# Optimization experiments

Measured on AMD Instinct MI355X. Metric: run time of the kernel, lower is better.

Reference implementation:

```python
import jax, jax.numpy as jnp
import numpy as np

QMAX = 127.0  # 2**(bits-1) - 1 for bits=8, signed symmetric


def _quantize_signed_symmetric(t):
    # per-tensor symmetric: scale = max|t| / qmax, q = clamp(round(t/scale))
    scale = jnp.max(jnp.abs(t)) / QMAX
    q = jnp.clip(jnp.round(t / scale), -QMAX, QMAX)
    return q, scale


def setup_inputs() -> dict:
    key = jax.random.key(0)
    k1, k2, k3 = jax.random.split(key, 3)
    N, D_IN, D_OUT = 16384, 1024, 1024
    x = jax.random.normal(k1, (N, D_IN), dtype=jnp.float32)
    weight = jax.random.normal(k2, (D_OUT, D_IN), dtype=jnp.float32) * 0.02
    bias = jax.random.normal(k3, (D_OUT,), dtype=jnp.float32) * 0.01
    return {"x": x, "weight": weight, "bias": bias}


def reference(x, weight, bias):
    # weight quantization (cached in torch; recomputed here, same math)
    qw, w_scale = _quantize_signed_symmetric(weight)
    qw_t = qw.astype(jnp.int32).T            # [D_IN, D_OUT]
    # activation quantization
    qx, x_scale = _quantize_signed_symmetric(x)
    qx = qx.astype(jnp.int32)                # [N, D_IN]
    # int32 matmul, then per-tensor dequant + bias
    acc = qx @ qw_t                          # int32 [N, D_OUT]
    y = acc.astype(jnp.float32) * (x_scale * w_scale)
    return y + bias
```

## Files before the change

### kernel.cpp

```cpp
#include <hip/hip_runtime.h>

#define QMAX 127.0f

typedef int int4v __attribute__((ext_vector_type(4)));
typedef float float4v __attribute__((ext_vector_type(4)));

__device__ __forceinline__ float amax4(float4 v) {
    return fmaxf(fmaxf(fabsf(v.x), fabsf(v.y)), fmaxf(fabsf(v.z), fabsf(v.w)));
}
__device__ __forceinline__ int qone(float v, float s) {
    float q = fminf(fmaxf(rintf(v / s), -QMAX), QMAX);
    return (int)q;
}
__device__ __forceinline__ int qpack4(float4 v, float s) {
    return (qone(v.x, s) & 255) | ((qone(v.y, s) & 255) << 8) |
           ((qone(v.z, s) & 255) << 16) | ((qone(v.w, s) & 255) << 24);
}

__global__ void absmax2_kernel(const float4* __restrict__ px, int n4x,
                               const float4* __restrict__ pw, int n4w,
                               int gx, int* __restrict__ amax) {
    const float4* p; int n4; int* out; int nb, bid;
    if ((int)blockIdx.x < gx) { p = px; n4 = n4x; out = amax + 0; nb = gx; bid = blockIdx.x; }
    else { p = pw; n4 = n4w; out = amax + 1; nb = gridDim.x - gx; bid = blockIdx.x - gx; }
    const int S = nb * blockDim.x;
    int i = bid * blockDim.x + threadIdx.x;
    float a = 0.f, b = 0.f, c = 0.f, d = 0.f;
    for (; i + 3 * S < n4; i += 4 * S) {
        float4 v0 = p[i];
        float4 v1 = p[i + S];
        float4 v2 = p[i + 2 * S];
        float4 v3 = p[i + 3 * S];
        a = fmaxf(a, amax4(v0));
        b = fmaxf(b, amax4(v1));
        c = fmaxf(c, amax4(v2));
        d = fmaxf(d, amax4(v3));
    }
    for (; i < n4; i += S) a = fmaxf(a, amax4(p[i]));
    float m = fmaxf(fmaxf(a, b), fmaxf(c, d));
    for (int off = 32; off; off >>= 1) m = fmaxf(m, __shfl_down(m, off, 64));
    __shared__ float sm[4];
    if ((threadIdx.x & 63) == 0) sm[threadIdx.x >> 6] = m;
    __syncthreads();
    if (threadIdx.x == 0) {
        float bm = fmaxf(fmaxf(sm[0], sm[1]), fmaxf(sm[2], sm[3]));
        atomicMax(out, (int)__float_as_uint(bm));
    }
}

__global__ void quantw_kernel(const float4* __restrict__ sw, int4v* __restrict__ dw,
                              int n16w, int kshift, int KC,
                              const int* __restrict__ amax) {
    const float scale = __uint_as_float((unsigned)amax[1]) / QMAX;
    const int stride = gridDim.x * blockDim.x;
    for (int i = blockIdx.x * blockDim.x + threadIdx.x; i < n16w; i += stride) {
        float4 v0 = sw[4 * i + 0];
        float4 v1 = sw[4 * i + 1];
        float4 v2 = sw[4 * i + 2];
        float4 v3 = sw[4 * i + 3];
        int4v o = { qpack4(v0, scale), qpack4(v1, scale),
                    qpack4(v2, scale), qpack4(v3, scale) };
        const int n = i >> kshift;
        const int kg = i & ((1 << kshift) - 1);
        const int kc = kg >> 2, q = kg & 3;
        const int g = n >> 4, r = n & 15;
        dw[(g * KC + kc) * 64 + q * 16 + r] = o;
    }
}

__global__ __launch_bounds__(1024, 4) void gemm_i8_kernel(
        const float* __restrict__ x, const char* __restrict__ qb,
        const float4* __restrict__ bias4, const int* __restrict__ amax,
        float* __restrict__ out, int M, int N, int K) {
    extern __shared__ char sA[];

    const int KC = K >> 6;
    const int CH = KC >> 2;
    const int tid = threadIdx.x;
    const int lane = tid & 63;
    const int wv = tid >> 6;
    const int m0 = blockIdx.x * 64;

    const int si = wv >> 2;
    const int skcl = wv & 3;
    const int srow = m0 + si * 16 + (lane & 15);
    const int sk0 = skcl * 64 + (lane >> 4) * 16;
    const float4* sbase4 = (const float4*)(x + (size_t)srow * K + sk0);
    const int sslot = si * 256 + skcl * 64 + lane;

    const float xs = __uint_as_float((unsigned)amax[0]) / QMAX;

    const char* bbase = qb + (size_t)(wv * 4) * KC * 1024 + lane * 16;

#define LOADB(Bb, kc)                                                        \
    do { _Pragma("unroll") for (int j = 0; j < 4; ++j)                       \
        Bb[j] = *(const int4v*)(bbase + ((size_t)j * KC + (kc)) * 1024);     \
    } while (0)
#define LOADA2(kcl, ih)                                                      \
    do { _Pragma("unroll") for (int i = 0; i < 2; ++i)                       \
        Af[i] = sAv[((ih) * 2 + i) * 256 + (kcl) * 64 + lane];               \
    } while (0)
#define MF2(Bb, ih)                                                          \
    do { _Pragma("unroll") for (int j = 0; j < 4; ++j)                       \
        _Pragma("unroll") for (int i = 0; i < 2; ++i)                        \
            acc[j][(ih) * 2 + i] = __builtin_amdgcn_mfma_i32_16x16x64_i8(    \
                Bb[j], Af[i], acc[j][(ih) * 2 + i], 0, 0, 0);                \
    } while (0)
#define KCQUAD(Bb0, Bb1, kcl0, kcl1)                                         \
    do { LOADA2(kcl0, 0); MF2(Bb0, 0); LOADA2(kcl0, 1); MF2(Bb0, 1);         \
         LOADA2(kcl1, 0); MF2(Bb1, 0); LOADA2(kcl1, 1); MF2(Bb1, 1);         \
    } while (0)
#define ISSUEA(h) do { xr0 = sbase4[(h) * 64]; xr1 = sbase4[(h) * 64 + 1]; } while (0)
#define ISSUEB(h) do { xr0 = sbase4[(h) * 64 + 2]; xr1 = sbase4[(h) * 64 + 3]; } while (0)

    float4 xr0, xr1;
    int qa0, qa1;
    int4v B0[4], B1[4], Af[2];

    ISSUEA(0);
    LOADB(B0, 0);
    qa0 = qpack4(xr0, xs); qa1 = qpack4(xr1, xs);
    ISSUEB(0);
    {
        int4v o = { qa0, qa1, qpack4(xr0, xs), qpack4(xr1, xs) };
        ((int4v*)sA)[sslot] = o;
    }
    __syncthreads();

    int4v acc[4][4];
    const int4v zero = {0, 0, 0, 0};
#pragma unroll
    for (int j = 0; j < 4; ++j)
#pragma unroll
        for (int i = 0; i < 4; ++i) acc[j][i] = zero;

#pragma unroll 1
    for (int h = 0; h < CH - 1; ++h) {
        const int4v* sAv = (const int4v*)(sA + (h & 1) * 16384);
        const int kc0 = h * 4;
        ISSUEA(h + 1);
        LOADB(B1, kc0 + 1);
        KCQUAD(B0, B1, 0, 1);
        LOADB(B0, kc0 + 2);
        qa0 = qpack4(xr0, xs); qa1 = qpack4(xr1, xs);
        ISSUEB(h + 1);
        LOADB(B1, kc0 + 3);
        KCQUAD(B0, B1, 2, 3);
        LOADB(B0, kc0 + 4);
        {
            int4v o = { qa0, qa1, qpack4(xr0, xs), qpack4(xr1, xs) };
            ((int4v*)(sA + ((h + 1) & 1) * 16384))[sslot] = o;
        }
        __syncthreads();
    }
    {
        const int4v* sAv = (const int4v*)(sA + ((CH - 1) & 1) * 16384);
        const int kc0 = (CH - 1) * 4;
        LOADB(B1, kc0 + 1);
        KCQUAD(B0, B1, 0, 1);
        LOADB(B0, kc0 + 2);
        LOADB(B1, kc0 + 3);
        KCQUAD(B0, B1, 2, 3);
    }

    const float sc = xs * (__uint_as_float((unsigned)amax[1]) / QMAX);
    const int quad = lane >> 4;
    const int rbase = m0 + (lane & 15);
    const int cb4 = wv * 16;
#pragma unroll
    for (int j = 0; j < 4; ++j) {
        const float4 bv = bias4[cb4 + j * 4 + quad];
#pragma unroll
        for (int i = 0; i < 4; ++i) {
            const int row = rbase + i * 16;
            float4v v;
            v[0] = (float)acc[j][i][0] * sc + bv.x;
            v[1] = (float)acc[j][i][1] * sc + bv.y;
            v[2] = (float)acc[j][i][2] * sc + bv.z;
            v[3] = (float)acc[j][i][3] * sc + bv.w;
            *((float4v*)(out + (size_t)row * N) + cb4 + j * 4 + quad) = v;
        }
    }
}

extern "C" void kernel_launch(void* const* d_in, const int* in_sizes, int n_in,
                              void* d_out, int out_size, void* d_ws, size_t ws_size,
                              hipStream_t stream) {
    const float* x = (const float*)d_in[0];
    const float* w = (const float*)d_in[1];
    const float* bias = (const float*)d_in[2];
    float* out = (float*)d_out;

    const int xn = in_sizes[0];
    const int wn = in_sizes[1];
    const int N = in_sizes[2];
    const int K = wn / N;
    const int M = xn / K;
    const int KC = K >> 6;
    const int kshift = __builtin_ctz(K >> 4);

    int* amax = (int*)d_ws;
    char* qw = (char*)d_ws + 1024;

    const int GAX = 2048, GAW = 256;
    absmax2_kernel<<<GAX + GAW, 256, 0, stream>>>(
        (const float4*)x, xn / 4, (const float4*)w, wn / 4, GAX, amax);

    quantw_kernel<<<256, 256, 0, stream>>>(
        (const float4*)w, (int4v*)qw, wn / 16, kshift, KC, amax);

    gemm_i8_kernel<<<M / 64, 1024, 32768, stream>>>(
        x, qw, (const float4*)bias, amax, out, M, N, K);
}
```

Baseline: 190.2 us.

## Halve waves per block and give each wave a 128-column output tile

The GEMM block drops from 16 waves to 8, and each wave now computes a 64x128 output tile (8x4 accumulators) in place of 64x64. The K staging step shrinks from 256 to 128 per LDS double-buffer stage, which halves shared memory. Each A fragment read from LDS now feeds 8 B fragments, so more MFMAs run per LDS load and per barrier. The cost is about twice the register pressure per wave and lower occupancy (launch bounds 512,2), which may reduce latency hiding for the global B loads.

```diff
diff --git a/kernel.cpp b/kernel.cpp
--- a/kernel.cpp
+++ b/kernel.cpp
@@ -68,54 +68,51 @@
     }
 }
 
-__global__ __launch_bounds__(1024, 4) void gemm_i8_kernel(
+__global__ __launch_bounds__(512, 2) void gemm_i8_kernel(
         const float* __restrict__ x, const char* __restrict__ qb,
         const float4* __restrict__ bias4, const int* __restrict__ amax,
         float* __restrict__ out, int M, int N, int K) {
     extern __shared__ char sA[];
 
     const int KC = K >> 6;
-    const int CH = KC >> 2;
+    const int NCH = KC >> 1;
     const int tid = threadIdx.x;
     const int lane = tid & 63;
     const int wv = tid >> 6;
     const int m0 = blockIdx.x * 64;
 
-    const int si = wv >> 2;
-    const int skcl = wv & 3;
+    const int si = wv >> 1;
+    const int skcl = wv & 1;
     const int srow = m0 + si * 16 + (lane & 15);
     const int sk0 = skcl * 64 + (lane >> 4) * 16;
     const float4* sbase4 = (const float4*)(x + (size_t)srow * K + sk0);
-    const int sslot = si * 256 + skcl * 64 + lane;
+    const int sslot = si * 128 + skcl * 64 + lane;
 
     const float xs = __uint_as_float((unsigned)amax[0]) / QMAX;
 
-    const char* bbase = qb + (size_t)(wv * 4) * KC * 1024 + lane * 16;
+    const char* bbase = qb + (size_t)(wv * 8) * KC * 1024 + lane * 16;
 
 #define LOADB(Bb, kc)                                                        \
-    do { _Pragma("unroll") for (int j = 0; j < 4; ++j)                       \
+    do { _Pragma("unroll") for (int j = 0; j < 8; ++j)                       \
         Bb[j] = *(const int4v*)(bbase + ((size_t)j * KC + (kc)) * 1024);     \
     } while (0)
-#define LOADA2(kcl, ih)                                                      \
-    do { _Pragma("unroll") for (int i = 0; i < 2; ++i)                       \
-        Af[i] = sAv[((ih) * 2 + i) * 256 + (kcl) * 64 + lane];               \
+#define LOADA(Af, buf, kcl)                                                  \
+    do { const int4v* sAv = (const int4v*)(sA + (buf) * 8192);               \
+        _Pragma("unroll") for (int i = 0; i < 4; ++i)                        \
+            Af[i] = sAv[i * 128 + (kcl) * 64 + lane];                        \
     } while (0)
-#define MF2(Bb, ih)                                                          \
-    do { _Pragma("unroll") for (int j = 0; j < 4; ++j)                       \
-        _Pragma("unroll") for (int i = 0; i < 2; ++i)                        \
-            acc[j][(ih) * 2 + i] = __builtin_amdgcn_mfma_i32_16x16x64_i8(    \
-                Bb[j], Af[i], acc[j][(ih) * 2 + i], 0, 0, 0);                \
+#define MF(Bb, Af)                                                           \
+    do { _Pragma("unroll") for (int j = 0; j < 8; ++j)                       \
+        _Pragma("unroll") for (int i = 0; i < 4; ++i)                        \
+            acc[j][i] = __builtin_amdgcn_mfma_i32_16x16x64_i8(               \
+                Bb[j], Af[i], acc[j][i], 0, 0, 0);                           \
     } while (0)
-#define KCQUAD(Bb0, Bb1, kcl0, kcl1)                                         \
-    do { LOADA2(kcl0, 0); MF2(Bb0, 0); LOADA2(kcl0, 1); MF2(Bb0, 1);         \
-         LOADA2(kcl1, 0); MF2(Bb1, 0); LOADA2(kcl1, 1); MF2(Bb1, 1);         \
-    } while (0)
-#define ISSUEA(h) do { xr0 = sbase4[(h) * 64]; xr1 = sbase4[(h) * 64 + 1]; } while (0)
-#define ISSUEB(h) do { xr0 = sbase4[(h) * 64 + 2]; xr1 = sbase4[(h) * 64 + 3]; } while (0)
+#define ISSUEA(h) do { xr0 = sbase4[(h) * 32]; xr1 = sbase4[(h) * 32 + 1]; } while (0)
+#define ISSUEB(h) do { xr0 = sbase4[(h) * 32 + 2]; xr1 = sbase4[(h) * 32 + 3]; } while (0)
 
     float4 xr0, xr1;
     int qa0, qa1;
-    int4v B0[4], B1[4], Af[2];
+    int4v B0[8], B1[8], Af[4];
 
     ISSUEA(0);
     LOADB(B0, 0);
@@ -127,48 +124,46 @@
     }
     __syncthreads();
 
-    int4v acc[4][4];
+    int4v acc[8][4];
     const int4v zero = {0, 0, 0, 0};
 #pragma unroll
-    for (int j = 0; j < 4; ++j)
+    for (int j = 0; j < 8; ++j)
 #pragma unroll
         for (int i = 0; i < 4; ++i) acc[j][i] = zero;
 
 #pragma unroll 1
-    for (int h = 0; h < CH - 1; ++h) {
-        const int4v* sAv = (const int4v*)(sA + (h & 1) * 16384);
-        const int kc0 = h * 4;
+    for (int h = 0; h < NCH - 1; ++h) {
+        const int kc0 = h * 2;
         ISSUEA(h + 1);
         LOADB(B1, kc0 + 1);
-        KCQUAD(B0, B1, 0, 1);
-        LOADB(B0, kc0 + 2);
+        LOADA(Af, h & 1, 0);
+        MF(B0, Af);
         qa0 = qpack4(xr0, xs); qa1 = qpack4(xr1, xs);
         ISSUEB(h + 1);
-        LOADB(B1, kc0 + 3);
-        KCQUAD(B0, B1, 2, 3);
-        LOADB(B0, kc0 + 4);
+        LOADB(B0, kc0 + 2);
+        LOADA(Af, h & 1, 1);
+        MF(B1, Af);
         {
             int4v o = { qa0, qa1, qpack4(xr0, xs), qpack4(xr1, xs) };
-            ((int4v*)(sA + ((h + 1) & 1) * 16384))[sslot] = o;
+            ((int4v*)(sA + ((h + 1) & 1) * 8192))[sslot] = o;
         }
         __syncthreads();
     }
     {
-        const int4v* sAv = (const int4v*)(sA + ((CH - 1) & 1) * 16384);
-        const int kc0 = (CH - 1) * 4;
+        const int kc0 = (NCH - 1) * 2;
         LOADB(B1, kc0 + 1);
-        KCQUAD(B0, B1, 0, 1);
-        LOADB(B0, kc0 + 2);
-        LOADB(B1, kc0 + 3);
-        KCQUAD(B0, B1, 2, 3);
+        LOADA(Af, (NCH - 1) & 1, 0);
+        MF(B0, Af);
+        LOADA(Af, (NCH - 1) & 1, 1);
+        MF(B1, Af);
     }
 
     const float sc = xs * (__uint_as_float((unsigned)amax[1]) / QMAX);
     const int quad = lane >> 4;
     const int rbase = m0 + (lane & 15);
-    const int cb4 = wv * 16;
-#pragma unroll
-    for (int j = 0; j < 4; ++j) {
+    const int cb4 = wv * 32;
+#pragma unroll
+    for (int j = 0; j < 8; ++j) {
         const float4 bv = bias4[cb4 + j * 4 + quad];
 #pragma unroll
         for (int i = 0; i < 4; ++i) {
@@ -209,6 +204,6 @@
     quantw_kernel<<<256, 256, 0, stream>>>(
         (const float4*)w, (int4v*)qw, wn / 16, kshift, KC, amax);
 
-    gemm_i8_kernel<<<M / 64, 1024, 32768, stream>>>(
+    gemm_i8_kernel<<<M / 64, 512, 16384, stream>>>(
         x, qw, (const float4*)bias, amax, out, M, N, K);
 }
```

Measured after the change: 178.5 us. 6.1% less time.
